# Performance work log

Measured on AMD Instinct MI355X. Metric: run time of the kernel, lower is better.

Reference implementation:

```python
import jax, jax.numpy as jnp
import numpy as np

B, S, D, H, HD, F = 8, 1024, 512, 8, 64, 2048
EPS = 1e-6

def rmsnorm(x, w):
    var = jnp.mean(x * x, axis=-1, keepdims=True)
    return w * (x * jax.lax.rsqrt(var + EPS))

def setup_inputs() -> dict:
    key = jax.random.key(0)
    ks = jax.random.split(key, 10)
    sd = 512 ** -0.5
    return {
        "primals_1": jax.random.normal(ks[0], (D, D), jnp.float32) * sd,
        "primals_2": jax.random.normal(ks[1], (D, D), jnp.float32) * sd,
        "primals_3": jax.random.normal(ks[2], (D, D), jnp.float32) * sd,
        "primals_4": jax.random.normal(ks[3], (D, D), jnp.float32) * sd,
        "primals_5": jax.random.uniform(ks[4], (D,), jnp.float32, 0.5, 1.5),
        "primals_6": jax.random.normal(ks[5], (F, D), jnp.float32) * sd,
        "primals_7": jax.random.normal(ks[6], (D, F), jnp.float32) * (F ** -0.5),
        "primals_8": jax.random.uniform(ks[7], (D,), jnp.float32, 0.5, 1.5),
        "primals_9": jax.random.normal(ks[8], (B, S, D), jnp.float32),
        "primals_10": jax.random.normal(ks[9], (B, H, S, S), jnp.float32) * 0.1,
    }

def reference(primals_1, primals_2, primals_3, primals_4, primals_5,
              primals_6, primals_7, primals_8, primals_9, primals_10):
    x = primals_9
    # --- self-attention sublayer ---
    h = rmsnorm(x, primals_5)                      # [B,S,D]
    # T5: no 1/sqrt(head_dim) scaling
    q = (h @ primals_3.T).reshape(B, S, H, HD).transpose(0, 2, 1, 3)  # [B,H,S,HD]
    k = (h @ primals_1.T).reshape(B, S, H, HD).transpose(0, 2, 1, 3)
    v = (h @ primals_4.T).reshape(B, S, H, HD).transpose(0, 2, 1, 3)
    scores = jnp.einsum('bhqd,bhkd->bhqk', q, k) + primals_10        # [B,H,S,S]
    attn = jax.nn.softmax(scores, axis=-1)
    ctx = jnp.einsum('bhqk,bhkd->bhqd', attn, v)                     # [B,H,S,HD]
    ctx = ctx.transpose(0, 2, 1, 3).reshape(B, S, D)
    x = x + ctx @ primals_2.T                       # residual add_1
    # --- FFN sublayer ---
    h2 = rmsnorm(x, primals_8)
    ff = jax.nn.relu(h2 @ primals_6.T)              # [B,S,F]
    out = x + ff @ primals_7.T                      # add_3
    return out
```

## Files before the change

### kernel.cpp

```cpp
#include <hip/hip_runtime.h>

#define B_ 8
#define S_ 1024
#define D_ 512
#define H_ 8
#define HD_ 64
#define F_ 2048

typedef unsigned short u16;
typedef unsigned int u32;
typedef __attribute__((ext_vector_type(8))) short bf16x8;
typedef __attribute__((ext_vector_type(4))) float f32x4;

__device__ __forceinline__ float bf2f(u16 u) {
  union { unsigned int i; float f; } v; v.i = ((unsigned int)u) << 16; return v.f;
}
__device__ __forceinline__ u16 f2bf(float f) {
  union { float f; unsigned int i; } v; v.f = f;
  unsigned int r = v.i + 0x7fffu + ((v.i >> 16) & 1u);
  return (u16)(r >> 16);
}

__device__ __forceinline__ void gl2lds16(const u16* g, u16* lds) {
  __builtin_amdgcn_global_load_lds(
      (const __attribute__((address_space(1))) unsigned int*)g,
      (__attribute__((address_space(3))) unsigned int*)lds, 16, 0, 0);
}

__global__ __launch_bounds__(256) void cvt_w_k(const float* __restrict__ wq, const float* __restrict__ wk,
                                               const float* __restrict__ wv, const float* __restrict__ wo,
                                               const float* __restrict__ wf1, const float* __restrict__ wf2,
                                               u16* __restrict__ dst) {
  size_t gid = (size_t)blockIdx.x * 256 + threadIdx.x;
  size_t e0 = gid * 4;
  const float* src; size_t loc;
  if      (e0 <  262144) { src = wq;  loc = e0; }
  else if (e0 <  524288) { src = wk;  loc = e0 -  262144; }
  else if (e0 <  786432) { src = wv;  loc = e0 -  524288; }
  else if (e0 < 1048576) { src = wo;  loc = e0 -  786432; }
  else if (e0 < 2097152) { src = wf1; loc = e0 - 1048576; }
  else                   { src = wf2; loc = e0 - 2097152; }
  float4 v = *(const float4*)(src + loc);
  ushort4 o; o.x = f2bf(v.x); o.y = f2bf(v.y); o.z = f2bf(v.z); o.w = f2bf(v.w);
  *(ushort4*)(dst + e0) = o;
}

template <int IN_BF16>
__global__ __launch_bounds__(256) void rmsnorm_k(const void* __restrict__ xv,
                                                 const float* __restrict__ w,
                                                 u16* __restrict__ out) {
  int row = blockIdx.x;
  int tid = threadIdx.x;
  float x0, x1;
  if (IN_BF16) {
    u32 v = ((const u32*)((const u16*)xv + (size_t)row * D_))[tid];
    x0 = bf2f((u16)(v & 0xffffu)); x1 = bf2f((u16)(v >> 16));
  } else {
    float2 v = ((const float2*)((const float*)xv + (size_t)row * D_))[tid];
    x0 = v.x; x1 = v.y;
  }
  float s = x0 * x0 + x1 * x1;
#pragma unroll
  for (int off = 32; off >= 1; off >>= 1) s += __shfl_xor(s, off, 64);
  __shared__ float red[4];
  int lane = tid & 63, wid = tid >> 6;
  if (lane == 0) red[wid] = s;
  __syncthreads();
  float tot = red[0] + red[1] + red[2] + red[3];
  float inv = rsqrtf(tot * (1.0f / D_) + 1e-6f);
  float2 wv = ((const float2*)w)[tid];
  u32 o = (u32)f2bf(x0 * inv * wv.x) | ((u32)f2bf(x1 * inv * wv.y) << 16);
  ((u32*)(out + (size_t)row * D_))[tid] = o;
}

template <int RELU, int RMODE, int OF32, int BM>
__global__ __launch_bounds__(256) void gemm_mfma_k(const u16* __restrict__ A,
                                                   const u16* __restrict__ W,
                                                   const void* __restrict__ Rv,
                                                   void* __restrict__ Cv,
                                                   int M, int N, int K) {
  constexpr int MI  = BM / 32;
  constexpr int ACH = BM / 16;
  __shared__ __align__(16) u16 As[BM * 32];
  __shared__ __align__(16) u16 Bs[128 * 32];
  int tid = threadIdx.x;
  int w = tid >> 6, l = tid & 63;
  int quad = l >> 4, l16 = l & 15;
  int m0 = blockIdx.y * BM, n0 = blockIdx.x * 128;
  int wr = (w >> 1) * (BM / 2), wc = (w & 1) * 64;

  int c_sw = (l & 3) ^ ((l >> 2) & 3);
  int r_in = l >> 2;
  int swz = quad ^ (l16 & 3);

  f32x4 acc[MI][4];
#pragma unroll
  for (int i = 0; i < MI; i++)
#pragma unroll
    for (int j = 0; j < 4; j++) acc[i][j] = (f32x4)(0.0f);

  for (int k0 = 0; k0 < K; k0 += 32) {
    __syncthreads();
#pragma unroll
    for (int t = 0; t < (ACH + 8) / 4; t++) {
      int ch = w * ((ACH + 8) / 4) + t;
      const u16* src; u16* dst;
      if (ch < ACH) { src = A + (size_t)(m0 + ch * 16 + r_in) * K;         dst = As + ch * 512; }
      else          { src = W + (size_t)(n0 + (ch - ACH) * 16 + r_in) * K; dst = Bs + (ch - ACH) * 512; }
      gl2lds16(src + k0 + c_sw * 8, dst);
    }
    __syncthreads();
    bf16x8 af[MI], bf[4];
#pragma unroll
    for (int i = 0; i < MI; i++)
      af[i] = *(const bf16x8*)(As + (wr + i * 16 + l16) * 32 + swz * 8);
#pragma unroll
    for (int j = 0; j < 4; j++)
      bf[j] = *(const bf16x8*)(Bs + (wc + j * 16 + l16) * 32 + swz * 8);
#pragma unroll
    for (int i = 0; i < MI; i++)
#pragma unroll
      for (int j = 0; j < 4; j++)
        acc[i][j] = __builtin_amdgcn_mfma_f32_16x16x32_bf16(af[i], bf[j], acc[i][j], 0, 0, 0);
  }

#pragma unroll
  for (int i = 0; i < MI; i++)
#pragma unroll
    for (int r = 0; r < 4; r++) {
      int mrow = m0 + wr + i * 16 + quad * 4 + r;
      size_t base = (size_t)mrow * N + n0 + wc + l16;
#pragma unroll
      for (int j = 0; j < 4; j++) {
        float v = acc[i][j][r];
        if (RELU) v = fmaxf(v, 0.0f);
        if (RMODE == 1) v += ((const float*)Rv)[base + j * 16];
        if (RMODE == 2) v += bf2f(((const u16*)Rv)[base + j * 16]);
        if (OF32) ((float*)Cv)[base + j * 16] = v;
        else      ((u16*)Cv)[base + j * 16]   = f2bf(v);
      }
    }
}

__global__ __launch_bounds__(256) void transpose_v_k(const u16* __restrict__ qkv,
                                                     u16* __restrict__ vt) {
  __shared__ u16 T[64][72];
  int t = threadIdx.x;
  int s0 = blockIdx.x * 64, h = blockIdx.y, b = blockIdx.z;
  int skey = t >> 3, dch = (t & 7) * 8;
  int rot = dch >> 3;
#pragma unroll
  for (int rnd = 0; rnd < 2; rnd++) {
    int s = s0 + skey + rnd * 32;
    bf16x8 vv = *(const bf16x8*)(qkv + ((size_t)(b * S_) + s) * 1536 + 1024 + h * HD_ + dch);
#pragma unroll
    for (int i = 0; i < 8; i++) {
      int ii = (i + rot) & 7;
      T[dch + ii][skey + rnd * 32] = (u16)((short*)&vv)[ii];
    }
  }
  __syncthreads();
  int d = t >> 2, kc = (t & 3) * 16;
  bf16x8 a0 = *(const bf16x8*)(&T[d][kc]);
  bf16x8 a1 = *(const bf16x8*)(&T[d][kc + 8]);
  u16* dst = vt + ((size_t)(b * H_ + h) * HD_ + d) * S_ + s0 + kc;
  *(bf16x8*)dst       = a0;
  *(bf16x8*)(dst + 8) = a1;
}

#define FIXED_M 20.0f

__device__ __forceinline__ void attn_stage(const u16* __restrict__ qkv,
                                           const u16* __restrict__ vt,
                                           u16* kvbuf, int b, int h, int kt,
                                           int w, int lane) {
#pragma unroll
  for (int i = 0; i < 2; i++) {
    int slot = w * 2 + i;
    int bufid = slot >> 2;
    int qq = slot & 3;
    int srow = qq * 16 + (lane >> 2);
    int slc = (lane & 3) ^ (srow & 3);
    const u16* src;
    if (bufid == 0)
      src = qkv + ((size_t)(b * S_) + kt + srow) * 1536 + 512 + h * HD_ + slc * 8;
    else if (bufid == 1)
      src = qkv + ((size_t)(b * S_) + kt + srow) * 1536 + 544 + h * HD_ + slc * 8;
    else if (bufid == 2)
      src = vt + ((size_t)((b * H_ + h) * HD_) + srow) * S_ + kt + slc * 8;
    else
      src = vt + ((size_t)((b * H_ + h) * HD_) + srow) * S_ + kt + 32 + slc * 8;
    gl2lds16(src, kvbuf + bufid * 2048 + qq * 512);
  }
}

__global__ __launch_bounds__(512, 4) void attn_v6_k(const u16* __restrict__ qkv,
                                                    const u16* __restrict__ vt,
                                                    const float* __restrict__ bias,
                                                    u16* __restrict__ ctx) {
  int tid = threadIdx.x;
  int w = tid >> 6, lane = tid & 63;
  int quad = lane >> 4, l16 = lane & 15;
  int h = blockIdx.y, b = blockIdx.z;
  int q0 = blockIdx.x * 128;

  __shared__ __align__(16) u16 KV[2][4 * 2048];
  __shared__ __align__(16) u16 Pl[8][16 * 72];

  const u16* qrow = qkv + ((size_t)(b * S_) + q0 + w * 16 + l16) * 1536 + h * HD_;
  bf16x8 qf0 = *(const bf16x8*)(qrow + quad * 8);
  bf16x8 qf1 = *(const bf16x8*)(qrow + 32 + quad * 8);

  float lr[4];
  f32x4 Oacc[4];
#pragma unroll
  for (int r = 0; r < 4; r++) lr[r] = 0.0f;
#pragma unroll
  for (int nt = 0; nt < 4; nt++) Oacc[nt] = (f32x4)(0.0f);

  const float* bpw = bias + ((size_t)((b * H_ + h) * S_) + q0 + w * 16) * S_;

  float bc[4][4], bn[4][4];
#pragma unroll
  for (int r = 0; r < 4; r++) {
    size_t bro = (size_t)(quad * 4 + r) * S_ + l16;
    bc[r][0] = bpw[bro];      bc[r][1] = bpw[bro + 16];
    bc[r][2] = bpw[bro + 32]; bc[r][3] = bpw[bro + 48];
  }

  int cur = 0;
  attn_stage(qkv, vt, &KV[0][0], b, h, 0, w, lane);

  for (int t = 0; t < 16; t++) {
    int kt = t * 64;
    __syncthreads();
    if (t < 15) {
      attn_stage(qkv, vt, &KV[cur ^ 1][0], b, h, kt + 64, w, lane);
#pragma unroll
      for (int r = 0; r < 4; r++) {
        size_t bro = (size_t)(quad * 4 + r) * S_ + kt + 64 + l16;
        bn[r][0] = bpw[bro];      bn[r][1] = bpw[bro + 16];
        bn[r][2] = bpw[bro + 32]; bn[r][3] = bpw[bro + 48];
      }
    }
    const u16* kvb = &KV[cur][0];

    f32x4 sg[4];
    __builtin_amdgcn_s_setprio(1);
#pragma unroll
    for (int g = 0; g < 4; g++) {
      int row = g * 16 + l16;
      int sw = quad ^ (row & 3);
      bf16x8 kf0 = *(const bf16x8*)(kvb + row * 32 + sw * 8);
      bf16x8 kf1 = *(const bf16x8*)(kvb + 2048 + row * 32 + sw * 8);
      f32x4 a = (f32x4)(0.0f);
      a = __builtin_amdgcn_mfma_f32_16x16x32_bf16(qf0, kf0, a, 0, 0, 0);
      a = __builtin_amdgcn_mfma_f32_16x16x32_bf16(qf1, kf1, a, 0, 0, 0);
      sg[g] = a;
    }
    __builtin_amdgcn_s_setprio(0);

#pragma unroll
    for (int r = 0; r < 4; r++) {
      float p0 = __expf(sg[0][r] + bc[r][0] - FIXED_M);
      float p1 = __expf(sg[1][r] + bc[r][1] - FIXED_M);
      float p2 = __expf(sg[2][r] + bc[r][2] - FIXED_M);
      float p3 = __expf(sg[3][r] + bc[r][3] - FIXED_M);
      lr[r] += (p0 + p1) + (p2 + p3);
      u16* prow = &Pl[w][(quad * 4 + r) * 72];
      prow[l16]      = f2bf(p0);
      prow[16 + l16] = f2bf(p1);
      prow[32 + l16] = f2bf(p2);
      prow[48 + l16] = f2bf(p3);
    }
    bf16x8 pf0 = *(const bf16x8*)(&Pl[w][l16 * 72 + quad * 8]);
    bf16x8 pf1 = *(const bf16x8*)(&Pl[w][l16 * 72 + 32 + quad * 8]);

    __builtin_amdgcn_s_setprio(1);
#pragma unroll
    for (int nt = 0; nt < 4; nt++) {
      int row = nt * 16 + l16;
      int sw = quad ^ (row & 3);
      bf16x8 vf0 = *(const bf16x8*)(kvb + 4096 + row * 32 + sw * 8);
      bf16x8 vf1 = *(const bf16x8*)(kvb + 6144 + row * 32 + sw * 8);
      Oacc[nt] = __builtin_amdgcn_mfma_f32_16x16x32_bf16(pf0, vf0, Oacc[nt], 0, 0, 0);
      Oacc[nt] = __builtin_amdgcn_mfma_f32_16x16x32_bf16(pf1, vf1, Oacc[nt], 0, 0, 0);
    }
    __builtin_amdgcn_s_setprio(0);

    if (t < 15) {
#pragma unroll
      for (int r = 0; r < 4; r++)
#pragma unroll
        for (int j = 0; j < 4; j++) bc[r][j] = bn[r][j];
    }
    cur ^= 1;
  }

  size_t obase = ((size_t)(b * S_) + q0 + w * 16) * D_ + h * HD_;
#pragma unroll
  for (int r = 0; r < 4; r++) {
    float s = lr[r];
    s += __shfl_xor(s, 1, 64);
    s += __shfl_xor(s, 2, 64);
    s += __shfl_xor(s, 4, 64);
    s += __shfl_xor(s, 8, 64);
    float inv = 1.0f / s;
    int qr = quad * 4 + r;
#pragma unroll
    for (int nt = 0; nt < 4; nt++) {
      ctx[obase + (size_t)qr * D_ + nt * 16 + l16] = f2bf(Oacc[nt][r] * inv);
    }
  }
}

extern "C" void kernel_launch(void* const* d_in, const int* in_sizes, int n_in,
                              void* d_out, int out_size, void* d_ws, size_t ws_size,
                              hipStream_t stream) {
  const float* Wk   = (const float*)d_in[0];
  const float* Wo   = (const float*)d_in[1];
  const float* Wq   = (const float*)d_in[2];
  const float* Wv   = (const float*)d_in[3];
  const float* g1   = (const float*)d_in[4];
  const float* Wf1  = (const float*)d_in[5];
  const float* Wf2  = (const float*)d_in[6];
  const float* g2   = (const float*)d_in[7];
  const float* X    = (const float*)d_in[8];
  const float* bias = (const float*)d_in[9];
  float* out = (float*)d_out;

  const size_t MD = (size_t)B_ * S_ * D_;
  u16* wbf   = (u16*)d_ws;
  u16* Wqkvb = wbf;
  u16* Wob   = wbf +  786432;
  u16* Wf1b  = wbf + 1048576;
  u16* Wf2b  = wbf + 2097152;
  u16* h     = wbf + 3145728;
  u16* qkv   = h + MD;
  u16* vtb   = qkv + 3 * MD;
  u16* ctx   = vtb + MD;
  u16* ff    = ctx + MD;
  u16* x1    = qkv;
  u16* h2    = h;

  dim3 blk(256);
  const int M = B_ * S_;

  cvt_w_k<<<3072, blk, 0, stream>>>(Wq, Wk, Wv, Wo, Wf1, Wf2, wbf);

  rmsnorm_k<0><<<M, blk, 0, stream>>>(X, g1, h);

  dim3 gqkv(1536 / 128, M / 128);
  gemm_mfma_k<0, 0, 0, 128><<<gqkv, blk, 0, stream>>>(h, Wqkvb, nullptr, qkv, M, 1536, D_);

  dim3 gt(S_ / 64, H_, B_);
  transpose_v_k<<<gt, blk, 0, stream>>>(qkv, vtb);

  dim3 ga(S_ / 128, H_, B_);
  attn_v6_k<<<ga, dim3(512), 0, stream>>>(qkv, vtb, bias, ctx);

  dim3 g512(D_ / 128, M / 128);
  gemm_mfma_k<0, 1, 0, 128><<<g512, blk, 0, stream>>>(ctx, Wob, X, x1, M, D_, D_);

  rmsnorm_k<1><<<M, blk, 0, stream>>>(x1, g2, h2);

  dim3 gff1(F_ / 128, M / 128);
  gemm_mfma_k<1, 0, 0, 128><<<gff1, blk, 0, stream>>>(h2, Wf1b, nullptr, ff, M, F_, D_);

  gemm_mfma_k<0, 2, 1, 128><<<g512, blk, 0, stream>>>(ff, Wf2b, x1, out, M, D_, F_);
}
```

Measured before the change: 575.1 us.

## Transpose QK MFMA so bias loads as float4 rows, two-deep prefetch

Swaps the MFMA operand order for the score product so each lane holds four consecutive key columns of one query row. This lets the bias be read with float4 loads instead of scalar strided loads. The bias is now prefetched two tiles ahead via unrolled ping-pong buffers, with an explicit vmcnt wait and raw s_barrier replacing __syncthreads. P is written to LDS as ushort4, and the row-sum reduction is restructured to match. The hand-tuned waitcnt counts risk correctness if the compiler reorders loads.

```diff
diff --git a/kernel.cpp b/kernel.cpp
--- a/kernel.cpp
+++ b/kernel.cpp
@@ -194,7 +194,7 @@
   }
 }
 
-__global__ __launch_bounds__(512, 4) void attn_v6_k(const u16* __restrict__ qkv,
+__global__ __launch_bounds__(512, 4) void attn_v7_k(const u16* __restrict__ qkv,
                                                     const u16* __restrict__ vt,
                                                     const float* __restrict__ bias,
                                                     u16* __restrict__ ctx) {
@@ -211,39 +211,25 @@
   bf16x8 qf0 = *(const bf16x8*)(qrow + quad * 8);
   bf16x8 qf1 = *(const bf16x8*)(qrow + 32 + quad * 8);
 
-  float lr[4];
+  float lr = 0.0f;
   f32x4 Oacc[4];
 #pragma unroll
-  for (int r = 0; r < 4; r++) lr[r] = 0.0f;
-#pragma unroll
   for (int nt = 0; nt < 4; nt++) Oacc[nt] = (f32x4)(0.0f);
 
-  const float* bpw = bias + ((size_t)((b * H_ + h) * S_) + q0 + w * 16) * S_;
-
-  float bc[4][4], bn[4][4];
-#pragma unroll
-  for (int r = 0; r < 4; r++) {
-    size_t bro = (size_t)(quad * 4 + r) * S_ + l16;
-    bc[r][0] = bpw[bro];      bc[r][1] = bpw[bro + 16];
-    bc[r][2] = bpw[bro + 32]; bc[r][3] = bpw[bro + 48];
-  }
-
-  int cur = 0;
+  const float* bln = bias + ((size_t)((b * H_ + h) * S_) + q0 + w * 16 + l16) * S_ + quad * 4;
+
+  float4 bb0[4], bb1[4];
+#pragma unroll
+  for (int g = 0; g < 4; g++) bb0[g] = *(const float4*)(bln + g * 16);
+#pragma unroll
+  for (int g = 0; g < 4; g++) bb1[g] = *(const float4*)(bln + 64 + g * 16);
+
   attn_stage(qkv, vt, &KV[0][0], b, h, 0, w, lane);
-
-  for (int t = 0; t < 16; t++) {
+  __syncthreads();
+
+  auto body = [&](int t, const u16* kvb, u16* kvnext, float4 (&bcur)[4]) {
     int kt = t * 64;
-    __syncthreads();
-    if (t < 15) {
-      attn_stage(qkv, vt, &KV[cur ^ 1][0], b, h, kt + 64, w, lane);
-#pragma unroll
-      for (int r = 0; r < 4; r++) {
-        size_t bro = (size_t)(quad * 4 + r) * S_ + kt + 64 + l16;
-        bn[r][0] = bpw[bro];      bn[r][1] = bpw[bro + 16];
-        bn[r][2] = bpw[bro + 32]; bn[r][3] = bpw[bro + 48];
-      }
-    }
-    const u16* kvb = &KV[cur][0];
+    if (t < 15) attn_stage(qkv, vt, kvnext, b, h, kt + 64, w, lane);
 
     f32x4 sg[4];
     __builtin_amdgcn_s_setprio(1);
@@ -254,25 +240,29 @@
       bf16x8 kf0 = *(const bf16x8*)(kvb + row * 32 + sw * 8);
       bf16x8 kf1 = *(const bf16x8*)(kvb + 2048 + row * 32 + sw * 8);
       f32x4 a = (f32x4)(0.0f);
-      a = __builtin_amdgcn_mfma_f32_16x16x32_bf16(qf0, kf0, a, 0, 0, 0);
-      a = __builtin_amdgcn_mfma_f32_16x16x32_bf16(qf1, kf1, a, 0, 0, 0);
+      a = __builtin_amdgcn_mfma_f32_16x16x32_bf16(kf0, qf0, a, 0, 0, 0);
+      a = __builtin_amdgcn_mfma_f32_16x16x32_bf16(kf1, qf1, a, 0, 0, 0);
       sg[g] = a;
     }
     __builtin_amdgcn_s_setprio(0);
 
 #pragma unroll
-    for (int r = 0; r < 4; r++) {
-      float p0 = __expf(sg[0][r] + bc[r][0] - FIXED_M);
-      float p1 = __expf(sg[1][r] + bc[r][1] - FIXED_M);
-      float p2 = __expf(sg[2][r] + bc[r][2] - FIXED_M);
-      float p3 = __expf(sg[3][r] + bc[r][3] - FIXED_M);
-      lr[r] += (p0 + p1) + (p2 + p3);
-      u16* prow = &Pl[w][(quad * 4 + r) * 72];
-      prow[l16]      = f2bf(p0);
-      prow[16 + l16] = f2bf(p1);
-      prow[32 + l16] = f2bf(p2);
-      prow[48 + l16] = f2bf(p3);
-    }
+    for (int g = 0; g < 4; g++) {
+      float4 bf = bcur[g];
+      float p0 = __expf(sg[g][0] + bf.x - FIXED_M);
+      float p1 = __expf(sg[g][1] + bf.y - FIXED_M);
+      float p2 = __expf(sg[g][2] + bf.z - FIXED_M);
+      float p3 = __expf(sg[g][3] + bf.w - FIXED_M);
+      lr += (p0 + p1) + (p2 + p3);
+      ushort4 pw;
+      pw.x = f2bf(p0); pw.y = f2bf(p1); pw.z = f2bf(p2); pw.w = f2bf(p3);
+      *(ushort4*)(&Pl[w][l16 * 72 + g * 16 + quad * 4]) = pw;
+    }
+    if (t < 14) {
+#pragma unroll
+      for (int g = 0; g < 4; g++) bcur[g] = *(const float4*)(bln + (size_t)(kt + 128) + g * 16);
+    }
+
     bf16x8 pf0 = *(const bf16x8*)(&Pl[w][l16 * 72 + quad * 8]);
     bf16x8 pf1 = *(const bf16x8*)(&Pl[w][l16 * 72 + 32 + quad * 8]);
 
@@ -288,24 +278,28 @@
     }
     __builtin_amdgcn_s_setprio(0);
 
-    if (t < 15) {
-#pragma unroll
-      for (int r = 0; r < 4; r++)
-#pragma unroll
-        for (int j = 0; j < 4; j++) bc[r][j] = bn[r][j];
-    }
-    cur ^= 1;
-  }
-
+    if (t < 14) {
+      asm volatile("s_waitcnt vmcnt(4)" ::: "memory");
+    } else {
+      asm volatile("s_waitcnt vmcnt(0)" ::: "memory");
+    }
+    __builtin_amdgcn_sched_barrier(0);
+    __builtin_amdgcn_s_barrier();
+  };
+
+#pragma unroll 1
+  for (int tt = 0; tt < 16; tt += 2) {
+    body(tt,     &KV[0][0], &KV[1][0], bb0);
+    body(tt + 1, &KV[1][0], &KV[0][0], bb1);
+  }
+
+  float s = lr;
+  s += __shfl_xor(s, 16, 64);
+  s += __shfl_xor(s, 32, 64);
   size_t obase = ((size_t)(b * S_) + q0 + w * 16) * D_ + h * HD_;
 #pragma unroll
   for (int r = 0; r < 4; r++) {
-    float s = lr[r];
-    s += __shfl_xor(s, 1, 64);
-    s += __shfl_xor(s, 2, 64);
-    s += __shfl_xor(s, 4, 64);
-    s += __shfl_xor(s, 8, 64);
-    float inv = 1.0f / s;
+    float inv = 1.0f / __shfl(s, quad * 4 + r, 64);
     int qr = quad * 4 + r;
 #pragma unroll
     for (int nt = 0; nt < 4; nt++) {
@@ -357,7 +351,7 @@
   transpose_v_k<<<gt, blk, 0, stream>>>(qkv, vtb);
 
   dim3 ga(S_ / 128, H_, B_);
-  attn_v6_k<<<ga, dim3(512), 0, stream>>>(qkv, vtb, bias, ctx);
+  attn_v7_k<<<ga, dim3(512), 0, stream>>>(qkv, vtb, bias, ctx);
 
   dim3 g512(D_ / 128, M / 128);
   gemm_mfma_k<0, 1, 0, 128><<<g512, blk, 0, stream>>>(ctx, Wob, X, x1, M, D_, D_);
```

After: 575.0 us. Within noise of the previous version (-0.0%).
